# Kernel tuning notes

Measured on AMD Instinct MI355X. Metric: run time of the kernel, lower is better.

Reference implementation:

```python
import jax, jax.numpy as jnp
import numpy as np

N, E, D, H, L = 10000, 80000, 1024, 8, 2
C = D // H          # 128 per-head channels
NEG = 0.2           # GATv2 default negative_slope


def setup_inputs() -> dict:
    k = jax.random.split(jax.random.key(0), 16)
    s = 0.02
    return {
        "x": jax.random.normal(k[0], (N, D), jnp.float32),
        "edge_index": jax.random.randint(k[1], (2, E), 0, N),
        "edge_attr": jax.random.randint(k[2], (E,), 0, 3),
        "node_types": jax.random.randint(k[3], (N,), 0, 5),
        "node_type_emb": s * jax.random.normal(k[4], (5, D), jnp.float32),
        "edge_type_emb": s * jax.random.normal(k[5], (3, D), jnp.float32),
        "Wl": s * jax.random.normal(k[6], (L, D, D), jnp.float32),
        "bl": jnp.zeros((L, D), jnp.float32),
        "Wr": s * jax.random.normal(k[7], (L, D, D), jnp.float32),
        "br": jnp.zeros((L, D), jnp.float32),
        "We": s * jax.random.normal(k[8], (L, D, D), jnp.float32),
        "att": s * jax.random.normal(k[9], (L, H, C), jnp.float32),
        "conv_bias": jnp.zeros((L, D), jnp.float32),
        "out_W": s * jax.random.normal(k[10], (D, D), jnp.float32),
        "out_b": jnp.zeros((D,), jnp.float32),
    }


def _gatv2(h, src, dst, ee, Wl, bl, Wr, br, We, att, b):
    """PyG GATv2Conv: concat=True, add_self_loops=True (fill_value='mean')."""
    n = h.shape[0]
    xl = (h @ Wl + bl).reshape(n, H, C)   # source transform (lin_l)
    xr = (h @ Wr + br).reshape(n, H, C)   # target transform (lin_r)
    # self loops: edge_attr of a loop = mean of raw incoming edge feats
    cnt = jax.ops.segment_sum(jnp.ones(src.shape, jnp.float32), dst, num_segments=n)
    loop_attr = jax.ops.segment_sum(ee, dst, num_segments=n) / jnp.maximum(cnt, 1.0)[:, None]
    loops = jnp.arange(n)
    s2 = jnp.concatenate([src, loops])
    d2 = jnp.concatenate([dst, loops])
    ea = jnp.concatenate([ee, loop_attr], axis=0)          # [E+N, D]
    ep = (ea @ We).reshape(-1, H, C)                        # lin_edge (no bias)
    e = jax.nn.leaky_relu(xl[s2] + xr[d2] + ep, NEG)        # [E+N, H, C]
    logit = jnp.einsum('ehc,hc->eh', e, att)                # attention logits
    # segment softmax over destination nodes (every node has a self loop)
    m = jax.ops.segment_max(logit, d2, num_segments=n)
    a = jnp.exp(logit - m[d2])
    alpha = a / jax.ops.segment_sum(a, d2, num_segments=n)[d2]
    out = jax.ops.segment_sum(alpha[:, :, None] * xl[s2], d2, num_segments=n)
    return out.reshape(n, D) + b


def reference(x, edge_index, edge_attr, node_types, node_type_emb, edge_type_emb,
              Wl, bl, Wr, br, We, att, conv_bias, out_W, out_b):
    h = x + node_type_emb[node_types]
    ee = edge_type_emb[edge_attr]
    src, dst = edge_index[0], edge_index[1]
    for i in range(L):  # num_layers = 2
        h = h + jax.nn.relu(_gatv2(h, src, dst, ee, Wl[i], bl[i], Wr[i], br[i],
                                   We[i], att[i], conv_bias[i]))
    return h @ out_W + out_b
```

## Files before the change

### kernel.cpp

```cpp
#include <hip/hip_runtime.h>
#include <hip/hip_bf16.h>
#include <stdint.h>

typedef __bf16 bf16_t;
typedef bf16_t bf16x8 __attribute__((ext_vector_type(8)));
typedef bf16_t bf16x4 __attribute__((ext_vector_type(4)));
typedef float f32x4 __attribute__((ext_vector_type(4)));

#define NN 10000
#define EE 80000
#define DD 1024
#define LL 2
#define MPAD 10112
#define NEGS 0.2f

#define GLOAD_LDS16(g, l) \
    __builtin_amdgcn_global_load_lds((__attribute__((address_space(1))) void*)(void*)(g), \
                                     (__attribute__((address_space(3))) void*)(l), 16, 0, 0)

__global__ __launch_bounds__(256)
void transpose_1024(const float* __restrict__ src, bf16_t* __restrict__ dstp)
{
    __shared__ float tile[32][33];
    int bx = blockIdx.x, by = blockIdx.y;
    int tx = threadIdx.x & 31, ty = threadIdx.x >> 5;
#pragma unroll
    for (int i = 0; i < 4; ++i)
        tile[ty + i*8][tx] = src[(size_t)(by*32 + ty + i*8)*1024 + bx*32 + tx];
    __syncthreads();
#pragma unroll
    for (int i = 0; i < 4; ++i)
        dstp[(size_t)(bx*32 + ty + i*8)*1024 + by*32 + tx] = (bf16_t)tile[tx][ty + i*8];
}

__global__ __launch_bounds__(256)
void h_init(const float* __restrict__ x, const int* __restrict__ ntypes,
            const float* __restrict__ nte, bf16_t* __restrict__ hbuf)
{
    size_t idx = ((size_t)blockIdx.x*256 + threadIdx.x) * 8;
    if (idx >= (size_t)MPAD*1024) return;
    int n = (int)(idx >> 10);
    int c = (int)(idx & 1023);
    bf16x8 outv;
    if (n < NN) {
        const float* xp = x + (size_t)n*1024 + c;
        int t = ntypes[n];
        const float* ep = nte + (size_t)t*1024 + c;
#pragma unroll
        for (int j = 0; j < 8; ++j) outv[j] = (bf16_t)(xp[j] + ep[j]);
    } else {
#pragma unroll
        for (int j = 0; j < 8; ++j) outv[j] = (bf16_t)0.f;
    }
    *(bf16x8*)(hbuf + idx) = outv;
}

__global__ void zero_i32(int* p, int n)
{ int i = blockIdx.x*256 + threadIdx.x; if (i < n) p[i] = 0; }

__global__ void zero_f32(float* p, int n)
{ int i = blockIdx.x*256 + threadIdx.x; if (i < n) p[i] = 0.f; }

__global__ void hist_k(const int* __restrict__ dsts, int* __restrict__ deg)
{ int e = blockIdx.x*256 + threadIdx.x; if (e < EE) atomicAdd(&deg[dsts[e]], 1); }

__global__ void scan_block(const int* __restrict__ deg, int* __restrict__ inc,
                           int* __restrict__ bsums)
{
    __shared__ int sdata[256];
    int i = blockIdx.x*256 + threadIdx.x;
    int v = (i < NN) ? deg[i] : 0;
    sdata[threadIdx.x] = v;
    __syncthreads();
    for (int d = 1; d < 256; d <<= 1) {
        int t = (threadIdx.x >= d) ? sdata[threadIdx.x - d] : 0;
        __syncthreads();
        sdata[threadIdx.x] += t;
        __syncthreads();
    }
    if (i < NN) inc[i] = sdata[threadIdx.x];
    if (threadIdx.x == 255) bsums[blockIdx.x] = sdata[255];
}

__global__ void scan_sums(int* bsums, int nb)
{
    if (threadIdx.x == 0 && blockIdx.x == 0) {
        int run = 0;
        for (int i = 0; i < nb; ++i) { int v = bsums[i]; bsums[i] = run; run += v; }
    }
}

__global__ void finalize_rp(const int* __restrict__ inc, const int* __restrict__ bsums,
                            int* __restrict__ rp)
{
    int i = blockIdx.x*256 + threadIdx.x;
    if (i < NN) rp[i+1] = inc[i] + bsums[i >> 8];
    if (i == 0) rp[0] = 0;
}

__global__ void copy_i32(const int* __restrict__ a, int* __restrict__ b, int n)
{ int i = blockIdx.x*256 + threadIdx.x; if (i < n) b[i] = a[i]; }

__global__ void fill_csr(const int* __restrict__ srcs, const int* __restrict__ dsts,
                         const int* __restrict__ etype, int* __restrict__ cursor,
                         int* __restrict__ sorted_src, int* __restrict__ sorted_typ)
{
    int e = blockIdx.x*256 + threadIdx.x;
    if (e < EE) {
        int d = dsts[e];
        int pos = atomicAdd(&cursor[d], 1);
        sorted_src[pos] = srcs[e];
        sorted_typ[pos] = etype[e];
    }
}

__global__ void pack_bias(const float* __restrict__ b1, const float* __restrict__ b2,
                          float* __restrict__ outb, int n1, int n2)
{
    int i = blockIdx.x*256 + threadIdx.x;
    if (i < n1) outb[i] = b1[i];
    else if (i < n1 + n2) outb[i] = b2[i - n1];
}

__global__ __launch_bounds__(256)
void compute_m3(const float* __restrict__ ete, const float* __restrict__ WeL,
                float* __restrict__ M3)
{
    int j  = (blockIdx.x & 3) * 256 + threadIdx.x;
    int k0 = (blockIdx.x >> 2) * 16;
    float a0 = 0.f, a1 = 0.f, a2 = 0.f;
#pragma unroll
    for (int kk = 0; kk < 16; ++kk) {
        int k = k0 + kk;
        float w = WeL[(size_t)k*1024 + j];
        a0 += ete[k]        * w;
        a1 += ete[1024 + k] * w;
        a2 += ete[2048 + k] * w;
    }
    atomicAdd(&M3[j],        a0);
    atomicAdd(&M3[1024 + j], a1);
    atomicAdd(&M3[2048 + j], a2);
}

template <typename OT>
__global__ __launch_bounds__(256)
void gemm_bt(const bf16_t* __restrict__ A, const bf16_t* __restrict__ BT,
             const float* __restrict__ bias, OT* __restrict__ Cmat,
             int K, int Ntot, int storeM, int mtiles, int ntiles)
{
    __shared__ __align__(16) bf16_t As[128*32];
    __shared__ __align__(16) bf16_t Bs[128*32];
    const int tid  = threadIdx.x;
    const int wave = tid >> 6;
    const int lane = tid & 63;

    const int GROUP_M = 8;
    int pid = blockIdx.x;
    int in_group = GROUP_M * ntiles;
    int gid = pid / in_group;
    int first_m = gid * GROUP_M;
    int gsz = mtiles - first_m; if (gsz > GROUP_M) gsz = GROUP_M;
    int local = pid % in_group;
    const int m0 = (first_m + (local % gsz)) * 128;
    const int n0 = (local / gsz) * 128;

    const int wm = (wave & 1) * 64;
    const int wn = (wave >> 1) * 64;
    const int quad = lane >> 4;
    const int l16  = lane & 15;
    const int srow = lane >> 2;
    const int skel = (lane & 3) * 8;

    f32x4 acc[4][4];
    f32x4 zero = {0.f, 0.f, 0.f, 0.f};
#pragma unroll
    for (int i = 0; i < 4; ++i)
#pragma unroll
        for (int j = 0; j < 4; ++j) acc[i][j] = zero;

    const bf16_t* aBase = A  + (size_t)(m0 + wave*32 + srow) * K + skel;
    const bf16_t* bBase = BT + (size_t)(n0 + wave*32 + srow) * K + skel;
    bf16_t* asDst = As + (wave*32)*32;
    bf16_t* bsDst = Bs + (wave*32)*32;

    for (int k0 = 0; k0 < K; k0 += 32) {
        GLOAD_LDS16(aBase + k0,                  asDst);
        GLOAD_LDS16(aBase + (size_t)16*K + k0,   asDst + 16*32);
        GLOAD_LDS16(bBase + k0,                  bsDst);
        GLOAD_LDS16(bBase + (size_t)16*K + k0,   bsDst + 16*32);
        __syncthreads();
        bf16x8 af[4], bfr[4];
#pragma unroll
        for (int mi = 0; mi < 4; ++mi)
            af[mi] = *(const bf16x8*)(As + (wm + mi*16 + l16)*32 + quad*8);
#pragma unroll
        for (int ni = 0; ni < 4; ++ni)
            bfr[ni] = *(const bf16x8*)(Bs + (wn + ni*16 + l16)*32 + quad*8);
#pragma unroll
        for (int mi = 0; mi < 4; ++mi)
#pragma unroll
            for (int ni = 0; ni < 4; ++ni)
                acc[mi][ni] = __builtin_amdgcn_mfma_f32_16x16x32_bf16(af[mi], bfr[ni], acc[mi][ni], 0, 0, 0);
        __syncthreads();
    }

#pragma unroll
    for (int mi = 0; mi < 4; ++mi) {
#pragma unroll
        for (int ni = 0; ni < 4; ++ni) {
            int col = n0 + wn + ni*16 + l16;
            float bv = bias[col];
#pragma unroll
            for (int r = 0; r < 4; ++r) {
                int row = m0 + wm + mi*16 + quad*4 + r;
                if (row < storeM)
                    Cmat[(size_t)row * Ntot + col] = (OT)(acc[mi][ni][r] + bv);
            }
        }
    }
}

__global__ __launch_bounds__(256)
void fused_edge(const int* __restrict__ rp, const int* __restrict__ ssrc,
                const int* __restrict__ styp, const bf16_t* __restrict__ XLXR,
                const float* __restrict__ M3, const float* __restrict__ attv,
                const float* __restrict__ cbias, bf16_t* __restrict__ hbuf)
{
    int node = blockIdx.x;
    int tid = threadIdx.x;
    int c = tid * 4;
    __shared__ int s_src[256];
    __shared__ int s_typ[256];

    int b = rp[node], en = rp[node + 1];

    bf16x4 xlv = *(const bf16x4*)(XLXR + (size_t)node*2048 + c);
    bf16x4 xrv = *(const bf16x4*)(XLXR + (size_t)node*2048 + 1024 + c);
    float xr0 = (float)xrv[0], xr1 = (float)xrv[1], xr2 = (float)xrv[2], xr3 = (float)xrv[3];
    float at0 = attv[c], at1 = attv[c+1], at2 = attv[c+2], at3 = attv[c+3];
    float m3r[3][4];
#pragma unroll
    for (int t = 0; t < 3; ++t)
#pragma unroll
        for (int j = 0; j < 4; ++j) m3r[t][j] = M3[t*1024 + c + j];

    float a0 = 0.f, a1 = 0.f, a2 = 0.f, a3 = 0.f;
    float den = 0.f;
    float cnt0 = 0.f, cnt1 = 0.f, cnt2 = 0.f;

    for (int base = b; base < en; base += 256) {
        int nchunk = en - base; if (nchunk > 256) nchunk = 256;
        __syncthreads();
        if (tid < nchunk) { s_src[tid] = ssrc[base + tid]; s_typ[tid] = styp[base + tid]; }
        __syncthreads();
        for (int i = 0; i < nchunk; ++i) {
            int s = s_src[i];
            int t = s_typ[i];
            bf16x4 xs = *(const bf16x4*)(XLXR + (size_t)s*2048 + c);
            float x0 = (float)xs[0], x1 = (float)xs[1], x2 = (float)xs[2], x3 = (float)xs[3];
            float v0 = x0 + xr0 + m3r[t][0]; v0 = (v0 > 0.f) ? v0 : NEGS * v0;
            float v1 = x1 + xr1 + m3r[t][1]; v1 = (v1 > 0.f) ? v1 : NEGS * v1;
            float v2 = x2 + xr2 + m3r[t][2]; v2 = (v2 > 0.f) ? v2 : NEGS * v2;
            float v3 = x3 + xr3 + m3r[t][3]; v3 = (v3 > 0.f) ? v3 : NEGS * v3;
            float part = v0*at0 + v1*at1 + v2*at2 + v3*at3;
            part += __shfl_xor(part, 1);
            part += __shfl_xor(part, 2);
            part += __shfl_xor(part, 4);
            part += __shfl_xor(part, 8);
            part += __shfl_xor(part, 16);
            part = fminf(fmaxf(part, -60.f), 60.f);
            float p = __expf(part);
            cnt0 += (t == 0) ? 1.f : 0.f;
            cnt1 += (t == 1) ? 1.f : 0.f;
            cnt2 += (t == 2) ? 1.f : 0.f;
            den += p;
            a0 += p * x0; a1 += p * x1; a2 += p * x2; a3 += p * x3;
        }
    }

    float deg = cnt0 + cnt1 + cnt2;
    float inv = 1.f / fmaxf(deg, 1.f);
    float w0 = cnt0 * inv, w1 = cnt1 * inv, w2 = cnt2 * inv;
    float sx0 = (float)xlv[0], sx1 = (float)xlv[1], sx2 = (float)xlv[2], sx3 = (float)xlv[3];
    float e0 = w0*m3r[0][0] + w1*m3r[1][0] + w2*m3r[2][0];
    float e1 = w0*m3r[0][1] + w1*m3r[1][1] + w2*m3r[2][1];
    float e2 = w0*m3r[0][2] + w1*m3r[1][2] + w2*m3r[2][2];
    float e3 = w0*m3r[0][3] + w1*m3r[1][3] + w2*m3r[2][3];
    float u0 = sx0 + xr0 + e0; u0 = (u0 > 0.f) ? u0 : NEGS * u0;
    float u1 = sx1 + xr1 + e1; u1 = (u1 > 0.f) ? u1 : NEGS * u1;
    float u2 = sx2 + xr2 + e2; u2 = (u2 > 0.f) ? u2 : NEGS * u2;
    float u3 = sx3 + xr3 + e3; u3 = (u3 > 0.f) ? u3 : NEGS * u3;
    float sp = u0*at0 + u1*at1 + u2*at2 + u3*at3;
    sp += __shfl_xor(sp, 1);
    sp += __shfl_xor(sp, 2);
    sp += __shfl_xor(sp, 4);
    sp += __shfl_xor(sp, 8);
    sp += __shfl_xor(sp, 16);
    sp = fminf(fmaxf(sp, -60.f), 60.f);
    float ps = __expf(sp);
    den += ps;
    a0 += ps * sx0; a1 += ps * sx1; a2 += ps * sx2; a3 += ps * sx3;

    float invd = 1.f / den;
    bf16x4 hv = *(const bf16x4*)(hbuf + (size_t)node*1024 + c);
    const float* cb = cbias + c;
    bf16x4 outv;
    outv[0] = (bf16_t)((float)hv[0] + fmaxf(a0*invd + cb[0], 0.f));
    outv[1] = (bf16_t)((float)hv[1] + fmaxf(a1*invd + cb[1], 0.f));
    outv[2] = (bf16_t)((float)hv[2] + fmaxf(a2*invd + cb[2], 0.f));
    outv[3] = (bf16_t)((float)hv[3] + fmaxf(a3*invd + cb[3], 0.f));
    *(bf16x4*)(hbuf + (size_t)node*1024 + c) = outv;
}

extern "C" void kernel_launch(void* const* d_in, const int* in_sizes, int n_in,
                              void* d_out, int out_size, void* d_ws, size_t ws_size,
                              hipStream_t stream)
{
    (void)in_sizes; (void)n_in; (void)out_size; (void)ws_size;
    const float* x     = (const float*)d_in[0];
    const int*   eidx  = (const int*)d_in[1];
    const int*   etype = (const int*)d_in[2];
    const int*   ntyp  = (const int*)d_in[3];
    const float* nte   = (const float*)d_in[4];
    const float* ete   = (const float*)d_in[5];
    const float* Wl    = (const float*)d_in[6];
    const float* bl    = (const float*)d_in[7];
    const float* Wr    = (const float*)d_in[8];
    const float* br    = (const float*)d_in[9];
    const float* We    = (const float*)d_in[10];
    const float* attw  = (const float*)d_in[11];
    const float* cbias = (const float*)d_in[12];
    const float* outW  = (const float*)d_in[13];
    const float* outb  = (const float*)d_in[14];
    const int* srcs = eidx;
    const int* dsts = eidx + EE;

    char* wsp = (char*)d_ws;
    size_t off = 0;
    auto carve = [&](size_t bytes) -> void* {
        void* pp = wsp + off;
        off += (bytes + 255) & ~(size_t)255;
        return pp;
    };
    bf16_t* hbuf  = (bf16_t*)carve((size_t)MPAD*1024*2);
    bf16_t* XLXR  = (bf16_t*)carve((size_t)MPAD*2048*2);
    bf16_t* WT    = (bf16_t*)carve((size_t)LL*2048*1024*2);
    bf16_t* OWT   = (bf16_t*)carve((size_t)1024*1024*2);
    float*  M3L   = (float*)carve((size_t)LL*3072*4);
    float*  biasb = (float*)carve(2048*4);
    int* deg    = (int*)carve((size_t)NN*4);
    int* rp     = (int*)carve((size_t)(NN+1)*4);
    int* cursor = (int*)carve((size_t)NN*4);
    int* ssrc   = (int*)carve((size_t)EE*4);
    int* styp   = (int*)carve((size_t)EE*4);
    int* incb   = (int*)carve((size_t)NN*4);
    int* bsums  = (int*)carve(64*4);

    dim3 tgrid(32, 32);
    for (int l = 0; l < LL; ++l) {
        transpose_1024<<<tgrid, 256, 0, stream>>>(Wl + (size_t)l*1024*1024, WT + (size_t)l*2048*1024);
        transpose_1024<<<tgrid, 256, 0, stream>>>(Wr + (size_t)l*1024*1024, WT + (size_t)l*2048*1024 + (size_t)1024*1024);
    }
    transpose_1024<<<tgrid, 256, 0, stream>>>(outW, OWT);

    h_init<<<5056, 256, 0, stream>>>(x, ntyp, nte, hbuf);

    zero_f32<<<(LL*3072 + 255)/256, 256, 0, stream>>>(M3L, LL*3072);
    for (int l = 0; l < LL; ++l)
        compute_m3<<<256, 256, 0, stream>>>(ete, We + (size_t)l*1024*1024, M3L + l*3072);

    zero_i32<<<40, 256, 0, stream>>>(deg, NN);
    hist_k<<<(EE + 255)/256, 256, 0, stream>>>(dsts, deg);
    scan_block<<<40, 256, 0, stream>>>(deg, incb, bsums);
    scan_sums<<<1, 64, 0, stream>>>(bsums, 40);
    finalize_rp<<<40, 256, 0, stream>>>(incb, bsums, rp);
    copy_i32<<<40, 256, 0, stream>>>(rp, cursor, NN);
    fill_csr<<<(EE + 255)/256, 256, 0, stream>>>(srcs, dsts, etype, cursor, ssrc, styp);

    for (int l = 0; l < LL; ++l) {
        pack_bias<<<8, 256, 0, stream>>>(bl + l*1024, br + l*1024, biasb, 1024, 1024);
        gemm_bt<bf16_t><<<79*16, 256, 0, stream>>>(hbuf, WT + (size_t)l*2048*1024, biasb, XLXR,
                                                   1024, 2048, MPAD, 79, 16);
        fused_edge<<<NN, 256, 0, stream>>>(rp, ssrc, styp, XLXR, M3L + l*3072, attw + l*1024,
                                           cbias + l*1024, hbuf);
    }

    pack_bias<<<4, 256, 0, stream>>>(outb, outb, biasb, 1024, 0);
    gemm_bt<float><<<79*8, 256, 0, stream>>>(hbuf, OWT, biasb, (float*)d_out,
                                             1024, 1024, NN, 79, 8);
}
```

Measured before the change: 451.8 us.

## Widen GEMM K-tile to 64 with XOR-swizzled LDS, batch transposes and bias packing

```diff
diff --git a/kernel.cpp b/kernel.cpp
--- a/kernel.cpp
+++ b/kernel.cpp
@@ -19,9 +19,21 @@
                                      (__attribute__((address_space(3))) void*)(l), 16, 0, 0)
 
 __global__ __launch_bounds__(256)
-void transpose_1024(const float* __restrict__ src, bf16_t* __restrict__ dstp)
+void transpose_batch(const float* __restrict__ Wl, const float* __restrict__ Wr,
+                     const float* __restrict__ outW,
+                     bf16_t* __restrict__ WT, bf16_t* __restrict__ OWT)
 {
     __shared__ float tile[32][33];
+    int z = blockIdx.z;
+    const float* src;
+    bf16_t* dstp;
+    switch (z) {
+        case 0: src = Wl;                       dstp = WT;                           break;
+        case 1: src = Wr;                       dstp = WT + (size_t)1024*1024;       break;
+        case 2: src = Wl + (size_t)1024*1024;   dstp = WT + (size_t)2*1024*1024;     break;
+        case 3: src = Wr + (size_t)1024*1024;   dstp = WT + (size_t)3*1024*1024;     break;
+        default: src = outW;                    dstp = OWT;                          break;
+    }
     int bx = blockIdx.x, by = blockIdx.y;
     int tx = threadIdx.x & 31, ty = threadIdx.x >> 5;
 #pragma unroll
@@ -114,12 +126,16 @@
     }
 }
 
-__global__ void pack_bias(const float* __restrict__ b1, const float* __restrict__ b2,
-                          float* __restrict__ outb, int n1, int n2)
+__global__ void pack_all_bias(const float* __restrict__ bl, const float* __restrict__ br,
+                              const float* __restrict__ outb, float* __restrict__ biasb)
 {
     int i = blockIdx.x*256 + threadIdx.x;
-    if (i < n1) outb[i] = b1[i];
-    else if (i < n1 + n2) outb[i] = b2[i - n1];
+    if (i < 4096) {
+        int l = i >> 11, j = i & 2047;
+        biasb[i] = (j < 1024) ? bl[l*1024 + j] : br[l*1024 + j - 1024];
+    } else if (i < 5120) {
+        biasb[i] = outb[i - 4096];
+    }
 }
 
 __global__ __launch_bounds__(256)
@@ -148,8 +164,8 @@
              const float* __restrict__ bias, OT* __restrict__ Cmat,
              int K, int Ntot, int storeM, int mtiles, int ntiles)
 {
-    __shared__ __align__(16) bf16_t As[128*32];
-    __shared__ __align__(16) bf16_t Bs[128*32];
+    __shared__ __align__(16) bf16_t As[128*64];
+    __shared__ __align__(16) bf16_t Bs[128*64];
     const int tid  = threadIdx.x;
     const int wave = tid >> 6;
     const int lane = tid & 63;
@@ -168,8 +184,9 @@
     const int wn = (wave >> 1) * 64;
     const int quad = lane >> 4;
     const int l16  = lane & 15;
-    const int srow = lane >> 2;
-    const int skel = (lane & 3) * 8;
+
+    const int srow = lane >> 3;
+    const int gcol = ((lane & 7) ^ srow) * 8;
 
     f32x4 acc[4][4];
     f32x4 zero = {0.f, 0.f, 0.f, 0.f};
@@ -178,29 +195,40 @@
 #pragma unroll
         for (int j = 0; j < 4; ++j) acc[i][j] = zero;
 
-    const bf16_t* aBase = A  + (size_t)(m0 + wave*32 + srow) * K + skel;
-    const bf16_t* bBase = BT + (size_t)(n0 + wave*32 + srow) * K + skel;
-    bf16_t* asDst = As + (wave*32)*32;
-    bf16_t* bsDst = Bs + (wave*32)*32;
-
-    for (int k0 = 0; k0 < K; k0 += 32) {
-        GLOAD_LDS16(aBase + k0,                  asDst);
-        GLOAD_LDS16(aBase + (size_t)16*K + k0,   asDst + 16*32);
-        GLOAD_LDS16(bBase + k0,                  bsDst);
-        GLOAD_LDS16(bBase + (size_t)16*K + k0,   bsDst + 16*32);
-        __syncthreads();
-        bf16x8 af[4], bfr[4];
-#pragma unroll
-        for (int mi = 0; mi < 4; ++mi)
-            af[mi] = *(const bf16x8*)(As + (wm + mi*16 + l16)*32 + quad*8);
-#pragma unroll
-        for (int ni = 0; ni < 4; ++ni)
-            bfr[ni] = *(const bf16x8*)(Bs + (wn + ni*16 + l16)*32 + quad*8);
-#pragma unroll
-        for (int mi = 0; mi < 4; ++mi)
-#pragma unroll
-            for (int ni = 0; ni < 4; ++ni)
-                acc[mi][ni] = __builtin_amdgcn_mfma_f32_16x16x32_bf16(af[mi], bfr[ni], acc[mi][ni], 0, 0, 0);
+    const bf16_t* aBase = A  + (size_t)(m0 + wave*8 + srow) * K + gcol;
+    const bf16_t* bBase = BT + (size_t)(n0 + wave*8 + srow) * K + gcol;
+    bf16_t* asDst = As + wave*512;
+    bf16_t* bsDst = Bs + wave*512;
+
+    for (int k0 = 0; k0 < K; k0 += 64) {
+#pragma unroll
+        for (int j = 0; j < 4; ++j)
+            GLOAD_LDS16(aBase + (size_t)(j*32)*K + k0, asDst + j*2048);
+#pragma unroll
+        for (int j = 0; j < 4; ++j)
+            GLOAD_LDS16(bBase + (size_t)(j*32)*K + k0, bsDst + j*2048);
+        __syncthreads();
+#pragma unroll
+        for (int kk = 0; kk < 2; ++kk) {
+            bf16x8 af[4], bfr[4];
+#pragma unroll
+            for (int mi = 0; mi < 4; ++mi) {
+                int row = wm + mi*16 + l16;
+                int ch  = ((kk*4 + quad) ^ (row & 7)) * 8;
+                af[mi] = *(const bf16x8*)(As + row*64 + ch);
+            }
+#pragma unroll
+            for (int ni = 0; ni < 4; ++ni) {
+                int row = wn + ni*16 + l16;
+                int ch  = ((kk*4 + quad) ^ (row & 7)) * 8;
+                bfr[ni] = *(const bf16x8*)(Bs + row*64 + ch);
+            }
+#pragma unroll
+            for (int mi = 0; mi < 4; ++mi)
+#pragma unroll
+                for (int ni = 0; ni < 4; ++ni)
+                    acc[mi][ni] = __builtin_amdgcn_mfma_f32_16x16x32_bf16(af[mi], bfr[ni], acc[mi][ni], 0, 0, 0);
+        }
         __syncthreads();
     }
 
@@ -347,7 +375,7 @@
     bf16_t* WT    = (bf16_t*)carve((size_t)LL*2048*1024*2);
     bf16_t* OWT   = (bf16_t*)carve((size_t)1024*1024*2);
     float*  M3L   = (float*)carve((size_t)LL*3072*4);
-    float*  biasb = (float*)carve(2048*4);
+    float*  biasb = (float*)carve(5120*4);
     int* deg    = (int*)carve((size_t)NN*4);
     int* rp     = (int*)carve((size_t)(NN+1)*4);
     int* cursor = (int*)carve((size_t)NN*4);
@@ -356,14 +384,9 @@
     int* incb   = (int*)carve((size_t)NN*4);
     int* bsums  = (int*)carve(64*4);
 
-    dim3 tgrid(32, 32);
-    for (int l = 0; l < LL; ++l) {
-        transpose_1024<<<tgrid, 256, 0, stream>>>(Wl + (size_t)l*1024*1024, WT + (size_t)l*2048*1024);
-        transpose_1024<<<tgrid, 256, 0, stream>>>(Wr + (size_t)l*1024*1024, WT + (size_t)l*2048*1024 + (size_t)1024*1024);
-    }
-    transpose_1024<<<tgrid, 256, 0, stream>>>(outW, OWT);
-
+    transpose_batch<<<dim3(32, 32, 5), 256, 0, stream>>>(Wl, Wr, outW, WT, OWT);
     h_init<<<5056, 256, 0, stream>>>(x, ntyp, nte, hbuf);
+    pack_all_bias<<<20, 256, 0, stream>>>(bl, br, outb, biasb);
 
     zero_f32<<<(LL*3072 + 255)/256, 256, 0, stream>>>(M3L, LL*3072);
     for (int l = 0; l < LL; ++l)
@@ -378,14 +401,13 @@
     fill_csr<<<(EE + 255)/256, 256, 0, stream>>>(srcs, dsts, etype, cursor, ssrc, styp);
 
     for (int l = 0; l < LL; ++l) {
-        pack_bias<<<8, 256, 0, stream>>>(bl + l*1024, br + l*1024, biasb, 1024, 1024);
-        gemm_bt<bf16_t><<<79*16, 256, 0, stream>>>(hbuf, WT + (size_t)l*2048*1024, biasb, XLXR,
+        gemm_bt<bf16_t><<<79*16, 256, 0, stream>>>(hbuf, WT + (size_t)l*2048*1024,
+                                                   biasb + l*2048, XLXR,
                                                    1024, 2048, MPAD, 79, 16);
         fused_edge<<<NN, 256, 0, stream>>>(rp, ssrc, styp, XLXR, M3L + l*3072, attw + l*1024,
                                            cbias + l*1024, hbuf);
     }
 
-    pack_bias<<<4, 256, 0, stream>>>(outb, outb, biasb, 1024, 0);
-    gemm_bt<float><<<79*8, 256, 0, stream>>>(hbuf, OWT, biasb, (float*)d_out,
+    gemm_bt<float><<<79*8, 256, 0, stream>>>(hbuf, OWT, biasb + 4096, (float*)d_out,
                                              1024, 1024, NN, 79, 8);
 }
```

After: 417.9 us. 7.5% less time.
